# Kernel optimization log

Measured on AMD Instinct MI355X. Metric: run time of the kernel, lower is better.

Reference implementation:

```python
import jax, jax.numpy as jnp
import numpy as np

B, Q, K, D = 8, 2048, 2048, 512

def setup_inputs() -> dict:
    key = jax.random.key(0)
    k1, k2, k3, k4, k5 = jax.random.split(key, 5)
    return {
        "query": jax.random.normal(k1, (B, Q, D), dtype=jnp.float32),
        "key": jax.random.normal(k2, (B, K, D), dtype=jnp.float32),
        "value": jax.random.normal(k3, (B, K, D), dtype=jnp.float32),
        "key_mask": jax.random.randint(k4, (B, K), 0, 2, dtype=jnp.int32),
        "W": jax.random.normal(k5, (D, D), dtype=jnp.float32) / np.sqrt(D),
    }

def reference(query, key, value, key_mask, W):
    # bilinear score: s[b,q,k] = query[b,q,:] @ W @ key[b,k,:]
    scale = 1.0 / jnp.sqrt(jnp.asarray(query.shape[-1], query.dtype))
    qW = jnp.einsum('bqd,de->bqe', query, W)          # [B,Q,D]
    scores = jnp.einsum('bqe,bke->bqk', qW, key)      # [B,Q,K]
    scores = jnp.where(key_mask[:, None, :] == 0, jnp.asarray(-1e20, scores.dtype), scores) * scale
    dist = jax.nn.softmax(scores, axis=-1)            # [B,Q,K]
    context = jnp.einsum('bqk,bkd->bqd', dist, value) # [B,Q,D]
    return context, dist
```

## Files before the change

kernel.cpp:

```cpp
#include <hip/hip_runtime.h>
#include <stdint.h>

#define BB 8
#define QQ 2048
#define KK 2048
#define DD 512

typedef _Float16 f16x8 __attribute__((ext_vector_type(8)));
typedef float f32x4 __attribute__((ext_vector_type(4)));

__device__ __forceinline__ unsigned short f2h(float f) {
    union { _Float16 h; unsigned short u; } x;
    x.h = (_Float16)f;
    return x.u;
}
__device__ __forceinline__ float h2f(unsigned short u) {
    union { unsigned short u; _Float16 h; } x;
    x.u = u;
    return (float)x.h;
}

__device__ __forceinline__ void async16(const unsigned short* g, unsigned short* l) {
    __builtin_amdgcn_global_load_lds(
        (const __attribute__((address_space(1))) unsigned int*)g,
        (__attribute__((address_space(3))) unsigned int*)l, 16, 0, 0);
}

__global__ __launch_bounds__(256) void cvt_f32_f16(const float* __restrict__ in,
                                                   unsigned short* __restrict__ out) {
    size_t i = ((size_t)blockIdx.x * 256 + threadIdx.x) * 8;
    float4 a = *(const float4*)(in + i);
    float4 b = *(const float4*)(in + i + 4);
    uint4 u;
    u.x = (unsigned)f2h(a.x) | ((unsigned)f2h(a.y) << 16);
    u.y = (unsigned)f2h(a.z) | ((unsigned)f2h(a.w) << 16);
    u.z = (unsigned)f2h(b.x) | ((unsigned)f2h(b.y) << 16);
    u.w = (unsigned)f2h(b.z) | ((unsigned)f2h(b.w) << 16);
    *(uint4*)(out + i) = u;
}

__global__ __launch_bounds__(256) void transpose_cvt(const float* __restrict__ in,
                                                     unsigned short* __restrict__ out,
                                                     int R, int C, long inB, long outB) {
    __shared__ float t[32][33];
    const float* ip = in + (size_t)blockIdx.z * inB;
    unsigned short* op = out + (size_t)blockIdx.z * outB;
    int x = threadIdx.x & 31, y0 = threadIdx.x >> 5;
    int c0 = blockIdx.x * 32, r0 = blockIdx.y * 32;
#pragma unroll
    for (int i = 0; i < 32; i += 8)
        t[y0 + i][x] = ip[(size_t)(r0 + y0 + i) * C + c0 + x];
    __syncthreads();
#pragma unroll
    for (int i = 0; i < 32; i += 8)
        op[(size_t)(c0 + y0 + i) * R + r0 + x] = f2h(t[x][y0 + i]);
}

template <int OUTM>
__global__ __launch_bounds__(256) void gemm_bt(const unsigned short* __restrict__ Aall,
                                               const unsigned short* __restrict__ Ball,
                                               void* __restrict__ Call,
                                               const int* __restrict__ maskAll,
                                               float* __restrict__ sums,
                                               int Kred, int lda, int ldb, int ldc,
                                               long aStride, long bStride, long cStride,
                                               int maskStride, float scale) {
    const int gx = gridDim.x, gy = gridDim.y;
    const int nwg = gx * gy * (int)gridDim.z;
    const int p = ((int)blockIdx.z * gy + (int)blockIdx.y) * gx + (int)blockIdx.x;
    const int qch = nwg >> 3, rch = nwg & 7;
    const int xcd = p & 7, ooff = p >> 3;
    const int w = (xcd < rch ? xcd * (qch + 1) : rch * (qch + 1) + (xcd - rch) * qch) + ooff;
    const int b = w / (gx * gy);
    const int rem = w - b * (gx * gy);
    const int my = rem / gx;
    const int nx = rem - my * gx;
    const int m0 = my * 128;
    const int n0 = nx * 128;

    __shared__ unsigned short As[128 * 32];
    __shared__ unsigned short Bs[128 * 32];

    const int tid = threadIdx.x;
    const int lane = tid & 63, wave = tid >> 6;
    const int wm = wave >> 1, wn = wave & 1;
    const int lrow = lane & 15, quad = lane >> 4;

    const int ar = tid >> 2, ac = (tid & 3) * 8;

    const unsigned short* Ab = Aall + (size_t)b * aStride + (size_t)m0 * lda;
    const unsigned short* Bb = Ball + (size_t)b * bStride + (size_t)n0 * ldb;
    unsigned short* AsW = As + wave * 512;
    unsigned short* BsW = Bs + wave * 512;

    f32x4 acc[4][4];
#pragma unroll
    for (int mi = 0; mi < 4; mi++)
#pragma unroll
        for (int ni = 0; ni < 4; ni++)
            acc[mi][ni] = (f32x4){0.f, 0.f, 0.f, 0.f};

    for (int kk = 0; kk < Kred; kk += 32) {
#pragma unroll
        for (int j = 0; j < 2; j++)
            async16(Ab + (size_t)(j * 64 + ar) * lda + kk + ac, AsW + j * 2048);
#pragma unroll
        for (int j = 0; j < 2; j++)
            async16(Bb + (size_t)(j * 64 + ar) * ldb + kk + ac, BsW + j * 2048);
        __syncthreads();

        f16x8 af[4], bfr[4];
#pragma unroll
        for (int i = 0; i < 4; i++)
            af[i] = *(const f16x8*)&As[(wm * 64 + i * 16 + lrow) * 32 + quad * 8];
#pragma unroll
        for (int i = 0; i < 4; i++)
            bfr[i] = *(const f16x8*)&Bs[(wn * 64 + i * 16 + lrow) * 32 + quad * 8];

#pragma unroll
        for (int mi = 0; mi < 4; mi++)
#pragma unroll
            for (int ni = 0; ni < 4; ni++)
                acc[mi][ni] = __builtin_amdgcn_mfma_f32_16x16x32_f16(af[mi], bfr[ni],
                                                                     acc[mi][ni], 0, 0, 0);
        __syncthreads();
    }

#pragma unroll
    for (int mi = 0; mi < 4; mi++) {
        const int gm = m0 + wm * 64 + mi * 16 + quad * 4;
        if constexpr (OUTM == 0) {
            unsigned short* C = (unsigned short*)Call + (size_t)b * cStride;
#pragma unroll
            for (int ni = 0; ni < 4; ni++) {
                int gn = n0 + wn * 64 + ni * 16 + lrow;
#pragma unroll
                for (int r = 0; r < 4; r++)
                    C[(size_t)(gm + r) * ldc + gn] = f2h(acc[mi][ni][r]);
            }
        } else {
            float* C = (float*)Call + (size_t)b * cStride;
            const float* s = sums + (size_t)b * QQ;
            float iv[4];
#pragma unroll
            for (int r = 0; r < 4; r++) iv[r] = 1.0f / s[gm + r];
#pragma unroll
            for (int ni = 0; ni < 4; ni++) {
                int gn = n0 + wn * 64 + ni * 16 + lrow;
#pragma unroll
                for (int r = 0; r < 4; r++)
                    C[(size_t)(gm + r) * ldc + gn] = acc[mi][ni][r] * iv[r];
            }
        }
    }
}

__global__ __launch_bounds__(512, 2) void gemm256_exp(
    const unsigned short* __restrict__ Aall, const unsigned short* __restrict__ Ball,
    unsigned short* __restrict__ Call, const int* __restrict__ maskAll,
    float* __restrict__ sums, int Kred, int lda, int ldb, int ldc,
    long aStride, long bStride, long cStride, int maskStride, float scale) {
    const int gx = gridDim.x, gy = gridDim.y;
    const int nwg = gx * gy * (int)gridDim.z;
    const int p = ((int)blockIdx.z * gy + (int)blockIdx.y) * gx + (int)blockIdx.x;
    const int qch = nwg >> 3, rch = nwg & 7;
    const int xcd = p & 7, ooff = p >> 3;
    const int w = (xcd < rch ? xcd * (qch + 1) : rch * (qch + 1) + (xcd - rch) * qch) + ooff;
    const int b = w / (gx * gy);
    const int rem = w - b * (gx * gy);
    const int my = rem / gx;
    const int nx = rem - my * gx;
    const int m0 = my * 256;
    const int n0 = nx * 256;

    __shared__ unsigned short As[4][256 * 32];
    __shared__ unsigned short Bs[4][256 * 32];

    const int tid = threadIdx.x;
    const int lane = tid & 63, wv = tid >> 6;
    const int wm = wv >> 2, wn = wv & 3;
    const int lrow = lane & 15, quad = lane >> 4;

    const int sr = lane >> 2;
    const int ssl = (lane & 3) ^ ((sr >> 1) & 3);
    const unsigned short* Ab = Aall + (size_t)b * aStride + (size_t)m0 * lda;
    const unsigned short* Bb = Ball + (size_t)b * bStride + (size_t)n0 * ldb;

    const int NT = Kred >> 5;

    auto stageA = [&](int t) {
#pragma unroll
        for (int j = 0; j < 2; j++) {
            const int c = wv * 2 + j;
            const int r = c * 16 + sr;
            async16(Ab + (size_t)r * lda + t * 32 + ssl * 8,
                    &As[t & 3][c * 512]);
        }
    };
    auto stageB = [&](int t) {
#pragma unroll
        for (int j = 0; j < 2; j++) {
            const int c = wv * 2 + j;
            const int r = c * 16 + sr;
            async16(Bb + (size_t)r * ldb + t * 32 + ssl * 8,
                    &Bs[t & 3][c * 512]);
        }
    };

    f32x4 acc[8][4];
#pragma unroll
    for (int mi = 0; mi < 8; mi++)
#pragma unroll
        for (int ni = 0; ni < 4; ni++)
            acc[mi][ni] = (f32x4){0.f, 0.f, 0.f, 0.f};

    for (int tt = 0; tt < 3 && tt < NT; ++tt) { stageA(tt); stageB(tt); }

    const int rsw = (lrow >> 1) & 3;

    for (int t = 0; t < NT; ++t) {
        if (t + 2 < NT)      asm volatile("s_waitcnt vmcnt(8)" ::: "memory");
        else if (t + 1 < NT) asm volatile("s_waitcnt vmcnt(4)" ::: "memory");
        else                 asm volatile("s_waitcnt vmcnt(0)" ::: "memory");
        __builtin_amdgcn_s_barrier();
        __builtin_amdgcn_sched_barrier(0);

        const unsigned short* Asl = As[t & 3];
        const unsigned short* Bsl = Bs[t & 3];
        f16x8 af[4], bfr[4];

        if (t + 3 < NT) stageA(t + 3);
#pragma unroll
        for (int ni = 0; ni < 4; ni++)
            bfr[ni] = *(const f16x8*)&Bsl[(wn * 64 + ni * 16 + lrow) * 32 + ((quad ^ rsw) * 8)];
#pragma unroll
        for (int mi = 0; mi < 4; mi++)
            af[mi] = *(const f16x8*)&Asl[(wm * 128 + mi * 16 + lrow) * 32 + ((quad ^ rsw) * 8)];
        __builtin_amdgcn_s_setprio(1);
#pragma unroll
        for (int mi = 0; mi < 4; mi++)
#pragma unroll
            for (int ni = 0; ni < 4; ni++)
                acc[mi][ni] = __builtin_amdgcn_mfma_f32_16x16x32_f16(af[mi], bfr[ni],
                                                                     acc[mi][ni], 0, 0, 0);
        __builtin_amdgcn_s_setprio(0);

        if (t + 3 < NT) stageB(t + 3);
#pragma unroll
        for (int mi = 0; mi < 4; mi++)
            af[mi] = *(const f16x8*)&Asl[(wm * 128 + (mi + 4) * 16 + lrow) * 32 + ((quad ^ rsw) * 8)];
        __builtin_amdgcn_s_setprio(1);
#pragma unroll
        for (int mi = 0; mi < 4; mi++)
#pragma unroll
            for (int ni = 0; ni < 4; ni++)
                acc[mi + 4][ni] = __builtin_amdgcn_mfma_f32_16x16x32_f16(af[mi], bfr[ni],
                                                                         acc[mi + 4][ni], 0, 0, 0);
        __builtin_amdgcn_s_setprio(0);
    }

    unsigned short* C = Call + (size_t)b * cStride;
    const int* mk = maskAll + (size_t)b * maskStride;
#pragma unroll
    for (int mi = 0; mi < 8; mi++) {
        const int gm = m0 + wm * 128 + mi * 16 + quad * 4;
        float ps[4] = {0.f, 0.f, 0.f, 0.f};
#pragma unroll
        for (int ni = 0; ni < 4; ni++) {
            int gn = n0 + wn * 64 + ni * 16 + lrow;
            bool keep = mk[gn] != 0;
#pragma unroll
            for (int r = 0; r < 4; r++) {
                float e = keep ? __expf(acc[mi][ni][r] * scale) : 0.f;
                C[(size_t)(gm + r) * ldc + gn] = f2h(e);
                ps[r] += e;
            }
        }
#pragma unroll
        for (int off = 1; off < 16; off <<= 1)
#pragma unroll
            for (int r = 0; r < 4; r++) ps[r] += __shfl_xor(ps[r], off);
        if (lrow == 0) {
            float* s = sums + (size_t)b * QQ;
#pragma unroll
            for (int r = 0; r < 4; r++) atomicAdd(&s[gm + r], ps[r]);
        }
    }
}

__global__ __launch_bounds__(256) void normalize_rows(const unsigned short* __restrict__ expS,
                                                      const float* __restrict__ sums,
                                                      float* __restrict__ dist) {
    const unsigned short* sp = expS + (size_t)blockIdx.x * 2048;
    float* dp = dist + (size_t)blockIdx.x * 2048;
    const float inv = 1.0f / sums[blockIdx.x];
    int tid = threadIdx.x;

    uint4 u = *(const uint4*)(sp + tid * 8);
    float4 o0, o1;
    o0.x = h2f((unsigned short)(u.x & 0xffff)) * inv;
    o0.y = h2f((unsigned short)(u.x >> 16)) * inv;
    o0.z = h2f((unsigned short)(u.y & 0xffff)) * inv;
    o0.w = h2f((unsigned short)(u.y >> 16)) * inv;
    o1.x = h2f((unsigned short)(u.z & 0xffff)) * inv;
    o1.y = h2f((unsigned short)(u.z >> 16)) * inv;
    o1.z = h2f((unsigned short)(u.w & 0xffff)) * inv;
    o1.w = h2f((unsigned short)(u.w >> 16)) * inv;
    *(float4*)(dp + tid * 8) = o0;
    *(float4*)(dp + tid * 8 + 4) = o1;
}

extern "C" void kernel_launch(void* const* d_in, const int* in_sizes, int n_in,
                              void* d_out, int out_size, void* d_ws, size_t ws_size,
                              hipStream_t stream) {
    const float* q    = (const float*)d_in[0];
    const float* k    = (const float*)d_in[1];
    const float* v    = (const float*)d_in[2];
    const int*   mask = (const int*)d_in[3];
    const float* W    = (const float*)d_in[4];

    float* ctx  = (float*)d_out;
    float* dist = ctx + (size_t)BB * QQ * DD;

    unsigned short* ws  = (unsigned short*)d_ws;
    unsigned short* Wt  = ws;
    unsigned short* Qh  = Wt + (size_t)DD * DD;
    unsigned short* Kh  = Qh + (size_t)BB * QQ * DD;
    unsigned short* Vt  = Kh + (size_t)BB * KK * DD;
    unsigned short* qWh = Vt + (size_t)BB * DD * KK;
    unsigned short* Sc  = qWh + (size_t)BB * QQ * DD;
    float* sums = (float*)(Sc + (size_t)BB * QQ * KK);

    const float scale = 0.044194173824159216f;

    (void)hipMemsetAsync(sums, 0, (size_t)BB * QQ * sizeof(float), stream);
    transpose_cvt<<<dim3(DD / 32, DD / 32, 1), 256, 0, stream>>>(W, Wt, DD, DD, 0, 0);
    cvt_f32_f16<<<dim3((BB * QQ * DD / 8) / 256), 256, 0, stream>>>(q, Qh);
    cvt_f32_f16<<<dim3((BB * KK * DD / 8) / 256), 256, 0, stream>>>(k, Kh);
    transpose_cvt<<<dim3(DD / 32, KK / 32, BB), 256, 0, stream>>>(
        v, Vt, KK, DD, (long)KK * DD, (long)DD * KK);
    gemm_bt<0><<<dim3(DD / 128, QQ / 128, BB), 256, 0, stream>>>(
        Qh, Wt, qWh, nullptr, nullptr, DD, DD, DD, DD,
        (long)QQ * DD, 0, (long)QQ * DD, 0, 0.f);
    gemm256_exp<<<dim3(KK / 256, QQ / 256, BB), 512, 0, stream>>>(
        qWh, Kh, Sc, mask, sums, DD, DD, DD, KK,
        (long)QQ * DD, (long)KK * DD, (long)QQ * KK, KK, scale);
    normalize_rows<<<dim3(BB * QQ), 256, 0, stream>>>(Sc, sums, dist);
    gemm_bt<2><<<dim3(DD / 128, QQ / 128, BB), 256, 0, stream>>>(
        Sc, Vt, ctx, nullptr, sums, KK, KK, KK, DD,
        (long)QQ * KK, (long)DD * KK, (long)QQ * DD, 0, 0.f);
}
```

Before: 414.1 us.

## Replace simple 128x128 GEMMs with pipelined 256x128 swizzled multi-buffer kernel

The qW projection and the context GEMM now use a new 512-thread kernel with 256x128 tiles. It keeps a 4-deep async global-to-LDS ring with three stages in flight, an XOR-swizzled LDS layout, split MFMA phases interleaved with prefetch, and s_setprio around the math. This is meant to hide global memory latency and avoid the two block-wide syncs per K step of the old single-buffer kernel, at the cost of more LDS and registers. The two f32-to-f16 conversions are also merged into one launch to save a kernel launch.

```diff
diff --git a/kernel.cpp b/kernel.cpp
--- a/kernel.cpp
+++ b/kernel.cpp
@@ -26,8 +26,12 @@
         (__attribute__((address_space(3))) unsigned int*)l, 16, 0, 0);
 }
 
-__global__ __launch_bounds__(256) void cvt_f32_f16(const float* __restrict__ in,
-                                                   unsigned short* __restrict__ out) {
+__global__ __launch_bounds__(256) void cvt_f32_f16_2(const float* __restrict__ in0,
+                                                     const float* __restrict__ in1,
+                                                     unsigned short* __restrict__ out0,
+                                                     unsigned short* __restrict__ out1) {
+    const float* in = blockIdx.y ? in1 : in0;
+    unsigned short* out = blockIdx.y ? out1 : out0;
     size_t i = ((size_t)blockIdx.x * 256 + threadIdx.x) * 8;
     float4 a = *(const float4*)(in + i);
     float4 b = *(const float4*)(in + i + 4);
@@ -57,14 +61,11 @@
 }
 
 template <int OUTM>
-__global__ __launch_bounds__(256) void gemm_bt(const unsigned short* __restrict__ Aall,
-                                               const unsigned short* __restrict__ Ball,
-                                               void* __restrict__ Call,
-                                               const int* __restrict__ maskAll,
-                                               float* __restrict__ sums,
-                                               int Kred, int lda, int ldb, int ldc,
-                                               long aStride, long bStride, long cStride,
-                                               int maskStride, float scale) {
+__global__ __launch_bounds__(512, 2) void gemm256n(
+    const unsigned short* __restrict__ Aall, const unsigned short* __restrict__ Ball,
+    void* __restrict__ Call, const float* __restrict__ sums,
+    int Kred, int lda, int ldb, int ldc,
+    long aStride, long bStride, long cStride) {
     const int gx = gridDim.x, gy = gridDim.y;
     const int nwg = gx * gy * (int)gridDim.z;
     const int p = ((int)blockIdx.z * gy + (int)blockIdx.y) * gx + (int)blockIdx.x;
@@ -75,65 +76,98 @@
     const int rem = w - b * (gx * gy);
     const int my = rem / gx;
     const int nx = rem - my * gx;
-    const int m0 = my * 128;
+    const int m0 = my * 256;
     const int n0 = nx * 128;
 
-    __shared__ unsigned short As[128 * 32];
-    __shared__ unsigned short Bs[128 * 32];
+    __shared__ unsigned short As[4][256 * 32];
+    __shared__ unsigned short Bs[4][128 * 32];
 
     const int tid = threadIdx.x;
-    const int lane = tid & 63, wave = tid >> 6;
-    const int wm = wave >> 1, wn = wave & 1;
+    const int lane = tid & 63, wv = tid >> 6;
+    const int wm = wv >> 2, wn = wv & 3;
     const int lrow = lane & 15, quad = lane >> 4;
 
-    const int ar = tid >> 2, ac = (tid & 3) * 8;
-
+    const int sr = lane >> 2;
+    const int ssl = (lane & 3) ^ ((sr >> 1) & 3);
     const unsigned short* Ab = Aall + (size_t)b * aStride + (size_t)m0 * lda;
     const unsigned short* Bb = Ball + (size_t)b * bStride + (size_t)n0 * ldb;
-    unsigned short* AsW = As + wave * 512;
-    unsigned short* BsW = Bs + wave * 512;
-
-    f32x4 acc[4][4];
-#pragma unroll
-    for (int mi = 0; mi < 4; mi++)
-#pragma unroll
-        for (int ni = 0; ni < 4; ni++)
+
+    const int NT = Kred >> 5;
+
+    auto stageA = [&](int t) {
+#pragma unroll
+        for (int j = 0; j < 2; j++) {
+            const int c = wv * 2 + j;
+            const int r = c * 16 + sr;
+            async16(Ab + (size_t)r * lda + t * 32 + ssl * 8, &As[t & 3][c * 512]);
+        }
+    };
+    auto stageB = [&](int t) {
+        const int c = wv;
+        const int r = c * 16 + sr;
+        async16(Bb + (size_t)r * ldb + t * 32 + ssl * 8, &Bs[t & 3][c * 512]);
+    };
+
+    f32x4 acc[8][2];
+#pragma unroll
+    for (int mi = 0; mi < 8; mi++)
+#pragma unroll
+        for (int ni = 0; ni < 2; ni++)
             acc[mi][ni] = (f32x4){0.f, 0.f, 0.f, 0.f};
 
-    for (int kk = 0; kk < Kred; kk += 32) {
-#pragma unroll
-        for (int j = 0; j < 2; j++)
-            async16(Ab + (size_t)(j * 64 + ar) * lda + kk + ac, AsW + j * 2048);
-#pragma unroll
-        for (int j = 0; j < 2; j++)
-            async16(Bb + (size_t)(j * 64 + ar) * ldb + kk + ac, BsW + j * 2048);
-        __syncthreads();
-
-        f16x8 af[4], bfr[4];
-#pragma unroll
-        for (int i = 0; i < 4; i++)
-            af[i] = *(const f16x8*)&As[(wm * 64 + i * 16 + lrow) * 32 + quad * 8];
-#pragma unroll
-        for (int i = 0; i < 4; i++)
-            bfr[i] = *(const f16x8*)&Bs[(wn * 64 + i * 16 + lrow) * 32 + quad * 8];
-
-#pragma unroll
-        for (int mi = 0; mi < 4; mi++)
-#pragma unroll
-            for (int ni = 0; ni < 4; ni++)
+    for (int tt = 0; tt < 3 && tt < NT; ++tt) { stageA(tt); stageB(tt); }
+
+    const int rsw = (lrow >> 1) & 3;
+
+    for (int t = 0; t < NT; ++t) {
+        if (t + 2 < NT)      asm volatile("s_waitcnt vmcnt(6)" ::: "memory");
+        else if (t + 1 < NT) asm volatile("s_waitcnt vmcnt(3)" ::: "memory");
+        else                 asm volatile("s_waitcnt vmcnt(0)" ::: "memory");
+        __builtin_amdgcn_s_barrier();
+        __builtin_amdgcn_sched_barrier(0);
+
+        const unsigned short* Asl = As[t & 3];
+        const unsigned short* Bsl = Bs[t & 3];
+        f16x8 af[4], bfr[2];
+
+        if (t + 3 < NT) stageA(t + 3);
+#pragma unroll
+        for (int ni = 0; ni < 2; ni++)
+            bfr[ni] = *(const f16x8*)&Bsl[(wn * 32 + ni * 16 + lrow) * 32 + ((quad ^ rsw) * 8)];
+#pragma unroll
+        for (int mi = 0; mi < 4; mi++)
+            af[mi] = *(const f16x8*)&Asl[(wm * 128 + mi * 16 + lrow) * 32 + ((quad ^ rsw) * 8)];
+        __builtin_amdgcn_s_setprio(1);
+#pragma unroll
+        for (int mi = 0; mi < 4; mi++)
+#pragma unroll
+            for (int ni = 0; ni < 2; ni++)
                 acc[mi][ni] = __builtin_amdgcn_mfma_f32_16x16x32_f16(af[mi], bfr[ni],
                                                                      acc[mi][ni], 0, 0, 0);
-        __syncthreads();
+        __builtin_amdgcn_s_setprio(0);
+
+        if (t + 3 < NT) stageB(t + 3);
+#pragma unroll
+        for (int mi = 0; mi < 4; mi++)
+            af[mi] = *(const f16x8*)&Asl[(wm * 128 + (mi + 4) * 16 + lrow) * 32 + ((quad ^ rsw) * 8)];
+        __builtin_amdgcn_s_setprio(1);
+#pragma unroll
+        for (int mi = 0; mi < 4; mi++)
+#pragma unroll
+            for (int ni = 0; ni < 2; ni++)
+                acc[mi + 4][ni] = __builtin_amdgcn_mfma_f32_16x16x32_f16(af[mi], bfr[ni],
+                                                                         acc[mi + 4][ni], 0, 0, 0);
+        __builtin_amdgcn_s_setprio(0);
     }
 
 #pragma unroll
-    for (int mi = 0; mi < 4; mi++) {
-        const int gm = m0 + wm * 64 + mi * 16 + quad * 4;
+    for (int mi = 0; mi < 8; mi++) {
+        const int gm = m0 + wm * 128 + mi * 16 + quad * 4;
         if constexpr (OUTM == 0) {
             unsigned short* C = (unsigned short*)Call + (size_t)b * cStride;
 #pragma unroll
-            for (int ni = 0; ni < 4; ni++) {
-                int gn = n0 + wn * 64 + ni * 16 + lrow;
+            for (int ni = 0; ni < 2; ni++) {
+                int gn = n0 + wn * 32 + ni * 16 + lrow;
 #pragma unroll
                 for (int r = 0; r < 4; r++)
                     C[(size_t)(gm + r) * ldc + gn] = f2h(acc[mi][ni][r]);
@@ -145,8 +179,8 @@
 #pragma unroll
             for (int r = 0; r < 4; r++) iv[r] = 1.0f / s[gm + r];
 #pragma unroll
-            for (int ni = 0; ni < 4; ni++) {
-                int gn = n0 + wn * 64 + ni * 16 + lrow;
+            for (int ni = 0; ni < 2; ni++) {
+                int gn = n0 + wn * 32 + ni * 16 + lrow;
 #pragma unroll
                 for (int r = 0; r < 4; r++)
                     C[(size_t)(gm + r) * ldc + gn] = acc[mi][ni][r] * iv[r];
@@ -193,8 +227,7 @@
         for (int j = 0; j < 2; j++) {
             const int c = wv * 2 + j;
             const int r = c * 16 + sr;
-            async16(Ab + (size_t)r * lda + t * 32 + ssl * 8,
-                    &As[t & 3][c * 512]);
+            async16(Ab + (size_t)r * lda + t * 32 + ssl * 8, &As[t & 3][c * 512]);
         }
     };
     auto stageB = [&](int t) {
@@ -202,8 +235,7 @@
         for (int j = 0; j < 2; j++) {
             const int c = wv * 2 + j;
             const int r = c * 16 + sr;
-            async16(Bb + (size_t)r * ldb + t * 32 + ssl * 8,
-                    &Bs[t & 3][c * 512]);
+            async16(Bb + (size_t)r * ldb + t * 32 + ssl * 8, &Bs[t & 3][c * 512]);
         }
     };
 
@@ -335,18 +367,17 @@
 
     (void)hipMemsetAsync(sums, 0, (size_t)BB * QQ * sizeof(float), stream);
     transpose_cvt<<<dim3(DD / 32, DD / 32, 1), 256, 0, stream>>>(W, Wt, DD, DD, 0, 0);
-    cvt_f32_f16<<<dim3((BB * QQ * DD / 8) / 256), 256, 0, stream>>>(q, Qh);
-    cvt_f32_f16<<<dim3((BB * KK * DD / 8) / 256), 256, 0, stream>>>(k, Kh);
+    cvt_f32_f16_2<<<dim3((BB * QQ * DD / 8) / 256, 2), 256, 0, stream>>>(q, k, Qh, Kh);
     transpose_cvt<<<dim3(DD / 32, KK / 32, BB), 256, 0, stream>>>(
         v, Vt, KK, DD, (long)KK * DD, (long)DD * KK);
-    gemm_bt<0><<<dim3(DD / 128, QQ / 128, BB), 256, 0, stream>>>(
-        Qh, Wt, qWh, nullptr, nullptr, DD, DD, DD, DD,
-        (long)QQ * DD, 0, (long)QQ * DD, 0, 0.f);
+    gemm256n<0><<<dim3(DD / 128, QQ / 256, BB), 512, 0, stream>>>(
+        Qh, Wt, qWh, nullptr, DD, DD, DD, DD,
+        (long)QQ * DD, 0, (long)QQ * DD);
     gemm256_exp<<<dim3(KK / 256, QQ / 256, BB), 512, 0, stream>>>(
         qWh, Kh, Sc, mask, sums, DD, DD, DD, KK,
         (long)QQ * DD, (long)KK * DD, (long)QQ * KK, KK, scale);
     normalize_rows<<<dim3(BB * QQ), 256, 0, stream>>>(Sc, sums, dist);
-    gemm_bt<2><<<dim3(DD / 128, QQ / 128, BB), 256, 0, stream>>>(
-        Sc, Vt, ctx, nullptr, sums, KK, KK, KK, DD,
-        (long)QQ * KK, (long)DD * KK, (long)QQ * DD, 0, 0.f);
-}
+    gemm256n<2><<<dim3(DD / 128, QQ / 256, BB), 512, 0, stream>>>(
+        Sc, Vt, ctx, sums, KK, KK, KK, DD,
+        (long)QQ * KK, (long)DD * KK, (long)QQ * DD);
+}
```

Result: no change. 418.9 us (+1.2%).
